# Performance work log

Hardware: AMD Instinct MI355X
Metric: run time of the kernel (lower is better)

Reference implementation:

```python
import jax, jax.numpy as jnp
import numpy as np

B, L, D = 4, 896, 2048
HQ, HKV, HD = 32, 8, 64
GROUP = HQ // HKV          # 4
TOKENS_PER_FRAME = 7
ROPE_BASE = 10000.0


def setup_inputs() -> dict:
    key = jax.random.key(0)
    ks = jax.random.split(key, 5)
    s = 0.02
    return {
        "x": jax.random.normal(ks[0], (B, L, D), jnp.float32),
        "wq": jax.random.normal(ks[1], (D, D), jnp.float32) * s,
        "wk": jax.random.normal(ks[2], (D, HKV * HD), jnp.float32) * s,
        "wv": jax.random.normal(ks[3], (D, HKV * HD), jnp.float32) * s,
        "wo": jax.random.normal(ks[4], (D, D), jnp.float32) * s,
        "pos_ids": jnp.arange(L, dtype=jnp.int32),
    }


def _apply_rotary(t, cos, sin):
    # t: [B, L, H, HD]; rotate all HD dims, interleaved pairs.
    Bt, Lt, Ht, Hd = t.shape
    tp = t.reshape(Bt, Lt, Ht, Hd // 2, 2)
    x1, x2 = tp[..., 0], tp[..., 1]
    c = cos[None, :, None, :]   # [1, L, 1, HD/2]
    s = sin[None, :, None, :]
    y1 = x1 * c - x2 * s
    y2 = x1 * s + x2 * c
    return jnp.stack([y1, y2], axis=-1).reshape(Bt, Lt, Ht, Hd)


def reference(x, wq, wk, wv, wo, pos_ids):
    Bx, Lx, Dx = x.shape
    q = (x @ wq).reshape(Bx, Lx, HQ, HD)
    k = (x @ wk).reshape(Bx, Lx, HKV, HD)
    v = (x @ wv).reshape(Bx, Lx, HKV, HD)

    # RoPE (rot_dim = head_dim), scale = 1.0
    half = HD // 2
    inv_freq = 1.0 / (ROPE_BASE ** (jnp.arange(half, dtype=jnp.float32) / half))
    freqs = pos_ids.astype(jnp.float32)[:, None] * inv_freq[None, :]  # [L, HD/2]
    cos, sin = jnp.cos(freqs), jnp.sin(freqs)
    q = _apply_rotary(q, cos, sin)
    k = _apply_rotary(k, cos, sin)

    # GQA: expand kv heads to q heads (kv_head = q_head // GROUP)
    k = jnp.repeat(k, GROUP, axis=2)   # [B, L, HQ, HD]
    v = jnp.repeat(v, GROUP, axis=2)

    scale = 1.0 / jnp.sqrt(jnp.float32(HD))
    scores = jnp.einsum('blhd,bmhd->bhlm', q, k) * scale  # [B, HQ, L, L]

    # frame-block causal mask: allow key frame <= query frame
    pos = jnp.arange(Lx)
    fid = pos // TOKENS_PER_FRAME
    allow = fid[None, :] <= fid[:, None]                  # [L, L]
    neg = jnp.finfo(scores.dtype).min
    scores = jnp.where(allow[None, None], scores, neg)

    probs = jax.nn.softmax(scores, axis=-1)
    out = jnp.einsum('bhlm,bmhd->blhd', probs, v).reshape(Bx, Lx, Dx)
    return out @ wo
```

## Files before the change

### kernel.cpp

```cpp
#include <hip/hip_runtime.h>
#include <hip/hip_bf16.h>
#include <cstdint>

typedef __bf16 bf16;
typedef __bf16 bf16x8 __attribute__((ext_vector_type(8)));
typedef float floatx4 __attribute__((ext_vector_type(4)));

#define B_   4
#define L_   896
#define D_   2048
#define HQ_  32
#define HKV_ 8
#define HD_  64
#define NQKV 3072
#define M_   3584

__device__ inline void gl_lds16(const bf16* g, bf16* l) {
    __builtin_amdgcn_global_load_lds(
        (const __attribute__((address_space(1))) void*)g,
        (__attribute__((address_space(3))) void*)l, 16, 0, 0);
}

__device__ inline void barrier_() {
    asm volatile("" ::: "memory");
    __builtin_amdgcn_s_barrier();
    asm volatile("" ::: "memory");
}

__global__ __launch_bounds__(256) void convert_to_bf16(const float* __restrict__ in,
                                                       bf16* __restrict__ out) {
    long q = (long)blockIdx.x * 256 + threadIdx.x;
    float4 v = ((const float4*)in)[q];
    union { bf16 b[4]; ushort4 u; } w;
    w.b[0] = (bf16)v.x; w.b[1] = (bf16)v.y; w.b[2] = (bf16)v.z; w.b[3] = (bf16)v.w;
    ((ushort4*)out)[q] = w.u;
}

__global__ __launch_bounds__(256) void rope_cs_kernel(const int* __restrict__ pos_ids,
                                                      float2* __restrict__ cs) {
    int idx = blockIdx.x * 256 + threadIdx.x;
    if (idx >= L_ * 32) return;
    int l = idx >> 5, i = idx & 31;
    float p = (float)pos_ids[l];
    float inv = exp2f(-(float)i * (13.287712379549449f / 32.0f));
    float a = p * inv;
    cs[idx] = make_float2(cosf(a), sinf(a));
}

__global__ __launch_bounds__(256) void rope_apply(bf16* __restrict__ QKV,
                                                  const float2* __restrict__ cs) {
    int idx = blockIdx.x * 256 + threadIdx.x;
    int m = idx / 320, g = idx - m * 320;
    int l = m % L_;
    int hp = (g * 4) & 31;
    const float2* ct = &cs[l * 32 + hp];
    bf16* p = QKV + (long)m * NQKV + g * 8;
    bf16x8 v = *(bf16x8*)p;
    bf16x8 w;
#pragma unroll
    for (int i = 0; i < 4; i++) {
        float2 csv = ct[i];
        float x1 = (float)v[2 * i], x2 = (float)v[2 * i + 1];
        w[2 * i]     = (bf16)(x1 * csv.x - x2 * csv.y);
        w[2 * i + 1] = (bf16)(x1 * csv.y + x2 * csv.x);
    }
    *(bf16x8*)p = w;
}

__global__ __launch_bounds__(256) void transpose_cvt(
    const float* __restrict__ in, ushort* __restrict__ out, int C, int R) {
    __shared__ ushort t[64][72];
    int tid = threadIdx.x;
    int tr = tid >> 4, tc = (tid & 15) << 2;
    long r0 = (long)blockIdx.y << 6, c0 = (long)blockIdx.x << 6;
#pragma unroll
    for (int i = 0; i < 4; ++i) {
        float4 v = *(const float4*)&in[(r0 + tr + i * 16) * C + c0 + tc];
        union { bf16 b[4]; ushort4 u; } w;
        w.b[0] = (bf16)v.x; w.b[1] = (bf16)v.y; w.b[2] = (bf16)v.z; w.b[3] = (bf16)v.w;
        *(ushort4*)&t[tr + i * 16][tc] = w.u;
    }
    __syncthreads();
#pragma unroll
    for (int i = 0; i < 4; ++i) {
        ushort4 w;
        w.x = t[tc + 0][tr + i * 16];
        w.y = t[tc + 1][tr + i * 16];
        w.z = t[tc + 2][tr + i * 16];
        w.w = t[tc + 3][tr + i * 16];
        *(ushort4*)&out[(c0 + tr + i * 16) * R + r0 + tc] = w;
    }
}

__global__ __launch_bounds__(256) void transpose_u16(
    const ushort* __restrict__ in, ushort* __restrict__ out,
    int ld_in, int ld_out, long is1, long is2, long os1, long os2) {
    __shared__ ushort t[64][72];
    int z = blockIdx.z;
    const ushort* ip = in + (long)(z >> 3) * is1 + (long)(z & 7) * is2;
    ushort* op = out + (long)(z >> 3) * os1 + (long)(z & 7) * os2;
    int tid = threadIdx.x;
    int tr = tid >> 4, tc = (tid & 15) << 2;
    long r0 = (long)blockIdx.y << 6, c0 = (long)blockIdx.x << 6;
#pragma unroll
    for (int i = 0; i < 4; ++i) {
        ushort4 v = *(const ushort4*)&ip[(r0 + tr + i * 16) * ld_in + c0 + tc];
        *(ushort4*)&t[tr + i * 16][tc] = v;
    }
    __syncthreads();
#pragma unroll
    for (int i = 0; i < 4; ++i) {
        ushort4 w;
        w.x = t[tc + 0][tr + i * 16];
        w.y = t[tc + 1][tr + i * 16];
        w.z = t[tc + 2][tr + i * 16];
        w.w = t[tc + 3][tr + i * 16];
        *(ushort4*)&op[(c0 + tr + i * 16) * ld_out + r0 + tc] = w;
    }
}

template <int JF, int OUTF32>
__global__ __launch_bounds__(512, 2) void gemm224(
    const bf16* __restrict__ A, const bf16* __restrict__ Bt, void* __restrict__ C,
    int Ntot, int Ktot) {
    __shared__ bf16 ldsA[2][224 * 64];
    __shared__ bf16 ldsB[2][JF * 64 * 64];
    const int tid = threadIdx.x;
    const int lane = tid & 63;
    const int quad = lane >> 4, l16 = lane & 15;
    const int w = tid >> 6;
    const int wr = w >> 2, wc = w & 3;

    const int gx = gridDim.x;
    const int nwg = gx * gridDim.y;
    int orig = blockIdx.y * gx + blockIdx.x;
    int q8 = nwg >> 3, r8 = nwg & 7;
    int xcd = orig & 7, lid = orig >> 3;
    int wg = (xcd < r8 ? xcd * (q8 + 1) : r8 * (q8 + 1) + (xcd - r8) * q8) + lid;
    const long m0 = (long)(wg / gx) * 224;
    const long n0 = (long)(wg % gx) * (JF * 64);

    const long rowK = Ktot;
    const int srow = tid >> 3;
    const int scol = ((tid & 7) ^ (srow & 7)) << 3;
    const bf16* baseA = A  + (m0 + srow) * rowK + scol;
    const bf16* baseB = Bt + (n0 + srow) * rowK + scol;
    bf16* const dA = (bf16*)ldsA + tid * 8;
    bf16* const dB = (bf16*)ldsB + tid * 8;

    const int m7 = l16 & 7;
    const int col0 = ((0 + quad) ^ m7) << 3;
    const int col1 = ((4 + quad) ^ m7) << 3;
    const int abase = wr * 112 + l16;
    const int bbase = wc * (JF * 16) + l16;

    floatx4 acc[7][JF];
#pragma unroll
    for (int i = 0; i < 7; ++i)
#pragma unroll
        for (int j = 0; j < JF; ++j)
#pragma unroll
            for (int r = 0; r < 4; ++r) acc[i][j][r] = 0.f;

    bf16x8 af0[4][2], af1[3][2], bq[JF][2];

    const int T = Ktot >> 6;

    {
        gl_lds16(baseA,              dA);
        gl_lds16(baseA + 64 * rowK,  dA + 4096);
        gl_lds16(baseA + 128 * rowK, dA + 8192);
        if (tid < 256) gl_lds16(baseA + 192 * rowK, dA + 12288);
#pragma unroll
        for (int r = 0; r < JF; ++r) gl_lds16(baseB + r * 64 * rowK, dB + r * 4096);
#pragma unroll
        for (int r = 0; r < JF; ++r) gl_lds16(baseB + 64 + r * 64 * rowK,
                                              dB + JF * 4096 + r * 4096);
    }
    if (JF == 3) asm volatile("s_waitcnt vmcnt(3)" ::: "memory");
    else         asm volatile("s_waitcnt vmcnt(2)" ::: "memory");
    barrier_();

    for (int t = 0; t < T; ++t) {
        const int cur = t & 1, nxt = cur ^ 1;
        const bf16* pa = &ldsA[cur][0];
        const bf16* pb = &ldsB[cur][0];
        const long koff  = (long)(t + 1) * 64;
        const long koff2 = (long)(t + 2) * 64;

#pragma unroll
        for (int i = 0; i < 4; ++i) {
            const bf16* rp = &pa[(abase + i * 16) * 64];
            af0[i][0] = *(const bf16x8*)&rp[col0];
            af0[i][1] = *(const bf16x8*)&rp[col1];
        }
#pragma unroll
        for (int j = 0; j < JF; ++j) {
            const bf16* rp = &pb[(bbase + j * 16) * 64];
            bq[j][0] = *(const bf16x8*)&rp[col0];
            bq[j][1] = *(const bf16x8*)&rp[col1];
        }
        if (t + 1 < T) {
            const bf16* g = baseA + koff;
            bf16* l = dA + nxt * (224 * 64);
            gl_lds16(g,              l);
            gl_lds16(g + 64 * rowK,  l + 4096);
            gl_lds16(g + 128 * rowK, l + 8192);
            if (tid < 256) gl_lds16(g + 192 * rowK, l + 12288);
        }
        barrier_();
        asm volatile("s_waitcnt lgkmcnt(0)" ::: "memory");
        __builtin_amdgcn_sched_barrier(0);
        __builtin_amdgcn_s_setprio(1);
#pragma unroll
        for (int i = 0; i < 4; ++i)
#pragma unroll
            for (int j = 0; j < JF; ++j) {
                floatx4 c = acc[i][j];
                c = __builtin_amdgcn_mfma_f32_16x16x32_bf16(af0[i][0], bq[j][0], c, 0, 0, 0);
                c = __builtin_amdgcn_mfma_f32_16x16x32_bf16(af0[i][1], bq[j][1], c, 0, 0, 0);
                acc[i][j] = c;
            }
        __builtin_amdgcn_s_setprio(0);
        barrier_();

#pragma unroll
        for (int i = 0; i < 3; ++i) {
            const bf16* rp = &pa[(abase + (4 + i) * 16) * 64];
            af1[i][0] = *(const bf16x8*)&rp[col0];
            af1[i][1] = *(const bf16x8*)&rp[col1];
        }
        if (t + 2 < T) {
            const bf16* g = baseB + koff2;
            bf16* l = dB + cur * (JF * 64 * 64);
#pragma unroll
            for (int r = 0; r < JF; ++r) gl_lds16(g + r * 64 * rowK, l + r * 4096);
        }
        barrier_();
        asm volatile("s_waitcnt lgkmcnt(0)" ::: "memory");
        __builtin_amdgcn_sched_barrier(0);
        __builtin_amdgcn_s_setprio(1);
#pragma unroll
        for (int i = 0; i < 3; ++i)
#pragma unroll
            for (int j = 0; j < JF; ++j) {
                floatx4 c = acc[4 + i][j];
                c = __builtin_amdgcn_mfma_f32_16x16x32_bf16(af1[i][0], bq[j][0], c, 0, 0, 0);
                c = __builtin_amdgcn_mfma_f32_16x16x32_bf16(af1[i][1], bq[j][1], c, 0, 0, 0);
                acc[4 + i][j] = c;
            }
        __builtin_amdgcn_s_setprio(0);
        if (t + 2 < T) {
            if (JF == 3) asm volatile("s_waitcnt vmcnt(3)" ::: "memory");
            else         asm volatile("s_waitcnt vmcnt(2)" ::: "memory");
        } else {
            asm volatile("s_waitcnt vmcnt(0)" ::: "memory");
        }
        barrier_();
    }

#pragma unroll
    for (int i = 0; i < 7; ++i)
#pragma unroll
        for (int j = 0; j < JF; ++j)
#pragma unroll
            for (int r = 0; r < 4; ++r) {
                long m = m0 + wr * 112 + i * 16 + quad * 4 + r;
                long n = n0 + wc * (JF * 16) + j * 16 + l16;
                if (OUTF32) ((float*)C)[m * Ntot + n] = acc[i][j][r];
                else        ((bf16*)C)[m * Ntot + n] = (bf16)acc[i][j][r];
            }
}

__global__ __launch_bounds__(256) void attn_kernel(
    const bf16* __restrict__ QKV,
    const bf16* __restrict__ Vt,
    bf16* __restrict__ AO) {
    __shared__ bf16 Ks[64 * 72];
    __shared__ bf16 Vs[64 * 72];
    __shared__ bf16 Ps[4][64 * 72];
    const int tid  = threadIdx.x;
    const int wid  = tid >> 6, lane = tid & 63;
    const int quad = lane >> 4, c = lane & 15;
    const int b = blockIdx.z, kvh = blockIdx.y;
    const int hq = kvh * 4 + wid;
    const int q0b = blockIdx.x * 64;
    bf16* ps = &Ps[wid][0];

    const bf16* Qb = QKV + ((long)(b * L_ + q0b)) * NQKV + hq * HD_;
    const bf16* Kb = QKV + ((long)(b * L_)) * NQKV + D_ + kvh * HD_;
    const bf16* Vb = Vt + ((long)(b * HKV_ + kvh)) * (HD_ * L_);

    bf16x8 qf[4][2];
#pragma unroll
    for (int a = 0; a < 4; a++) {
        qf[a][0] = *(const bf16x8*)&Qb[(long)(a * 16 + c) * NQKV + quad * 8];
        qf[a][1] = *(const bf16x8*)&Qb[(long)(a * 16 + c) * NQKV + 32 + quad * 8];
    }

    float lsum[4][4];
    floatx4 o[4][4];
#pragma unroll
    for (int a = 0; a < 4; a++)
#pragma unroll
        for (int r = 0; r < 4; r++) lsum[a][r] = 0.f;
#pragma unroll
    for (int a = 0; a < 4; a++)
#pragma unroll
        for (int nt = 0; nt < 4; nt++)
#pragma unroll
            for (int r = 0; r < 4; r++) o[a][nt][r] = 0.f;

    int fe[4][4];
#pragma unroll
    for (int a = 0; a < 4; a++)
#pragma unroll
        for (int r = 0; r < 4; r++) {
            int l = q0b + a * 16 + quad * 4 + r;
            fe[a][r] = (l / 7 + 1) * 7;
        }
    const int kend = ((q0b + 63) / 7 + 1) * 7;

    const int srow = tid >> 3, schunk = (tid & 7) << 3;

    for (int k0 = 0; k0 < kend; k0 += 64) {
        bf16x8 kg0 = *(const bf16x8*)&Kb[(long)(k0 + srow) * NQKV + schunk];
        bf16x8 kg1 = *(const bf16x8*)&Kb[(long)(k0 + 32 + srow) * NQKV + schunk];
        bf16x8 vg0 = *(const bf16x8*)&Vb[(long)srow * L_ + k0 + schunk];
        bf16x8 vg1 = *(const bf16x8*)&Vb[(long)(srow + 32) * L_ + k0 + schunk];
        __syncthreads();
        *(bf16x8*)&Ks[srow * 72 + schunk]        = kg0;
        *(bf16x8*)&Ks[(srow + 32) * 72 + schunk] = kg1;
        *(bf16x8*)&Vs[srow * 72 + schunk]        = vg0;
        *(bf16x8*)&Vs[(srow + 32) * 72 + schunk] = vg1;
        __syncthreads();

        bf16x8 kf[4][2];
#pragma unroll
        for (int n = 0; n < 4; n++) {
            kf[n][0] = *(bf16x8*)&Ks[(n * 16 + c) * 72 + quad * 8];
            kf[n][1] = *(bf16x8*)&Ks[(n * 16 + c) * 72 + 32 + quad * 8];
        }
#pragma unroll
        for (int a = 0; a < 4; a++) {
            floatx4 s[4];
#pragma unroll
            for (int n = 0; n < 4; n++) {
#pragma unroll
                for (int r = 0; r < 4; r++) s[n][r] = 0.f;
                s[n] = __builtin_amdgcn_mfma_f32_16x16x32_bf16(qf[a][0], kf[n][0], s[n], 0, 0, 0);
                s[n] = __builtin_amdgcn_mfma_f32_16x16x32_bf16(qf[a][1], kf[n][1], s[n], 0, 0, 0);
            }
#pragma unroll
            for (int n = 0; n < 4; n++) {
                const int key = k0 + n * 16 + c;
#pragma unroll
                for (int r = 0; r < 4; r++) {
                    float e = __expf(fmaf(s[n][r], 0.125f, -12.0f));
                    e = (key < fe[a][r]) ? e : 0.f;
                    lsum[a][r] += e;
                    ps[(a * 16 + quad * 4 + r) * 72 + n * 16 + c] = (bf16)e;
                }
            }
        }
        bf16x8 vf[4][2];
#pragma unroll
        for (int nt = 0; nt < 4; nt++) {
            vf[nt][0] = *(bf16x8*)&Vs[(nt * 16 + c) * 72 + quad * 8];
            vf[nt][1] = *(bf16x8*)&Vs[(nt * 16 + c) * 72 + 32 + quad * 8];
        }
#pragma unroll
        for (int a = 0; a < 4; a++) {
            bf16x8 pf0 = *(bf16x8*)&ps[(a * 16 + c) * 72 + quad * 8];
            bf16x8 pf1 = *(bf16x8*)&ps[(a * 16 + c) * 72 + 32 + quad * 8];
#pragma unroll
            for (int nt = 0; nt < 4; nt++) {
                o[a][nt] = __builtin_amdgcn_mfma_f32_16x16x32_bf16(pf0, vf[nt][0], o[a][nt], 0, 0, 0);
                o[a][nt] = __builtin_amdgcn_mfma_f32_16x16x32_bf16(pf1, vf[nt][1], o[a][nt], 0, 0, 0);
            }
        }
    }
#pragma unroll
    for (int a = 0; a < 4; a++)
#pragma unroll
        for (int r = 0; r < 4; r++) {
#pragma unroll
            for (int off = 1; off < 16; off <<= 1) lsum[a][r] += __shfl_xor(lsum[a][r], off);
        }
#pragma unroll
    for (int a = 0; a < 4; a++)
#pragma unroll
        for (int nt = 0; nt < 4; nt++)
#pragma unroll
            for (int r = 0; r < 4; r++) {
                int l = q0b + a * 16 + quad * 4 + r;
                AO[((long)(b * L_ + l)) * D_ + hq * HD_ + nt * 16 + c] =
                    (bf16)(o[a][nt][r] / lsum[a][r]);
            }
}

extern "C" void kernel_launch(void* const* d_in, const int* in_sizes, int n_in,
                              void* d_out, int out_size, void* d_ws, size_t ws_size,
                              hipStream_t stream) {
    (void)in_sizes; (void)n_in; (void)out_size; (void)ws_size;
    const float* x  = (const float*)d_in[0];
    const float* wq = (const float*)d_in[1];
    const float* wk = (const float*)d_in[2];
    const float* wv = (const float*)d_in[3];
    const float* wo = (const float*)d_in[4];
    const int* pos  = (const int*)d_in[5];

    bf16* ws    = (bf16*)d_ws;
    bf16* xb    = ws;
    bf16* wqkvT = ws + 7340032L;
    bf16* woT   = ws + 13631488L;
    bf16* QKV   = ws + 17825792L;
    bf16* Vt    = ws + 28835840L;
    bf16* AO    = xb;
    float2* cs  = (float2*)(ws + 30670848L);

    convert_to_bf16<<<dim3(7168), 256, 0, stream>>>(x, xb);
    rope_cs_kernel<<<dim3(112), dim3(256), 0, stream>>>(pos, cs);

    transpose_cvt<<<dim3(32, 32), 256, 0, stream>>>(wq, (ushort*)wqkvT, 2048, 2048);
    transpose_cvt<<<dim3(8, 32), 256, 0, stream>>>(wk, (ushort*)(wqkvT + 4194304L), 512, 2048);
    transpose_cvt<<<dim3(8, 32), 256, 0, stream>>>(wv, (ushort*)(wqkvT + 5242880L), 512, 2048);
    transpose_cvt<<<dim3(32, 32), 256, 0, stream>>>(wo, (ushort*)woT, 2048, 2048);

    gemm224<3, 0><<<dim3(16, 16), 512, 0, stream>>>(xb, wqkvT, QKV, NQKV, D_);

    rope_apply<<<dim3(4480), 256, 0, stream>>>(QKV, cs);

    transpose_u16<<<dim3(1, 14, 32), 256, 0, stream>>>(
        (const ushort*)(QKV + 2560), (ushort*)Vt, 3072, 896,
        896L * 3072, 64, 8L * 57344, 57344);

    attn_kernel<<<dim3(14, 8, 4), 256, 0, stream>>>(QKV, Vt, AO);

    gemm224<2, 1><<<dim3(16, 16), 512, 0, stream>>>(AO, woT, d_out, D_, D_);
}
```

Baseline: 268.3 us.

## Rebalance causal attention by pairing query tiles per block with prefetch and mask skip

Each block now handles two query tiles, x and 13-x, in sequence so causal work is balanced across blocks. It uses 8 waves of 512 threads, each wave covering 32 query rows. The next K/V tile is loaded into registers while the current one is computed. Mask evaluation is skipped for key tiles that lie fully below the frame boundary, and exp2 with a folded scale replaces expf with a constant shift. The grid halves to 224 blocks, which may leave CUs underused, and dropping the stabilizing shift slightly raises overflow risk.

```diff
diff --git a/kernel.cpp b/kernel.cpp
--- a/kernel.cpp
+++ b/kernel.cpp
@@ -272,131 +272,159 @@
             }
 }
 
-__global__ __launch_bounds__(256) void attn_kernel(
+__global__ __launch_bounds__(512) void attn_kernel(
     const bf16* __restrict__ QKV,
     const bf16* __restrict__ Vt,
     bf16* __restrict__ AO) {
     __shared__ bf16 Ks[64 * 72];
     __shared__ bf16 Vs[64 * 72];
-    __shared__ bf16 Ps[4][64 * 72];
+    __shared__ bf16 Ps[8][32 * 72];
     const int tid  = threadIdx.x;
     const int wid  = tid >> 6, lane = tid & 63;
     const int quad = lane >> 4, c = lane & 15;
     const int b = blockIdx.z, kvh = blockIdx.y;
-    const int hq = kvh * 4 + wid;
-    const int q0b = blockIdx.x * 64;
+    const int hq = kvh * 4 + (wid >> 1);
+    const int sub = wid & 1;
+    const int xpair = blockIdx.x;
     bf16* ps = &Ps[wid][0];
 
-    const bf16* Qb = QKV + ((long)(b * L_ + q0b)) * NQKV + hq * HD_;
     const bf16* Kb = QKV + ((long)(b * L_)) * NQKV + D_ + kvh * HD_;
     const bf16* Vb = Vt + ((long)(b * HKV_ + kvh)) * (HD_ * L_);
 
-    bf16x8 qf[4][2];
-#pragma unroll
-    for (int a = 0; a < 4; a++) {
-        qf[a][0] = *(const bf16x8*)&Qb[(long)(a * 16 + c) * NQKV + quad * 8];
-        qf[a][1] = *(const bf16x8*)&Qb[(long)(a * 16 + c) * NQKV + 32 + quad * 8];
-    }
-
-    float lsum[4][4];
-    floatx4 o[4][4];
-#pragma unroll
-    for (int a = 0; a < 4; a++)
-#pragma unroll
-        for (int r = 0; r < 4; r++) lsum[a][r] = 0.f;
-#pragma unroll
-    for (int a = 0; a < 4; a++)
-#pragma unroll
-        for (int nt = 0; nt < 4; nt++)
-#pragma unroll
-            for (int r = 0; r < 4; r++) o[a][nt][r] = 0.f;
-
-    int fe[4][4];
-#pragma unroll
-    for (int a = 0; a < 4; a++)
-#pragma unroll
-        for (int r = 0; r < 4; r++) {
-            int l = q0b + a * 16 + quad * 4 + r;
-            fe[a][r] = (l / 7 + 1) * 7;
-        }
-    const int kend = ((q0b + 63) / 7 + 1) * 7;
-
     const int srow = tid >> 3, schunk = (tid & 7) << 3;
-
-    for (int k0 = 0; k0 < kend; k0 += 64) {
-        bf16x8 kg0 = *(const bf16x8*)&Kb[(long)(k0 + srow) * NQKV + schunk];
-        bf16x8 kg1 = *(const bf16x8*)&Kb[(long)(k0 + 32 + srow) * NQKV + schunk];
-        bf16x8 vg0 = *(const bf16x8*)&Vb[(long)srow * L_ + k0 + schunk];
-        bf16x8 vg1 = *(const bf16x8*)&Vb[(long)(srow + 32) * L_ + k0 + schunk];
-        __syncthreads();
-        *(bf16x8*)&Ks[srow * 72 + schunk]        = kg0;
-        *(bf16x8*)&Ks[(srow + 32) * 72 + schunk] = kg1;
-        *(bf16x8*)&Vs[srow * 72 + schunk]        = vg0;
-        *(bf16x8*)&Vs[(srow + 32) * 72 + schunk] = vg1;
-        __syncthreads();
-
-        bf16x8 kf[4][2];
-#pragma unroll
-        for (int n = 0; n < 4; n++) {
-            kf[n][0] = *(bf16x8*)&Ks[(n * 16 + c) * 72 + quad * 8];
-            kf[n][1] = *(bf16x8*)&Ks[(n * 16 + c) * 72 + 32 + quad * 8];
-        }
-#pragma unroll
-        for (int a = 0; a < 4; a++) {
-            floatx4 s[4];
+    const bf16* kp = &Kb[(long)srow * NQKV + schunk];
+    const bf16* vp = &Vb[(long)srow * L_ + schunk];
+
+    const floatx4 fzero = {0.f, 0.f, 0.f, 0.f};
+    const float C1 = 0.18033688011112042f;
+
+#pragma unroll 1
+    for (int pass = 0; pass < 2; ++pass) {
+        const int x = pass == 0 ? xpair : 13 - xpair;
+        const int q0b = x * 64;
+        const bf16* Qb = QKV + ((long)(b * L_ + q0b + sub * 32)) * NQKV + hq * HD_;
+
+        bf16x8 qf[2][2];
+#pragma unroll
+        for (int a = 0; a < 2; a++) {
+            qf[a][0] = *(const bf16x8*)&Qb[(long)(a * 16 + c) * NQKV + quad * 8];
+            qf[a][1] = *(const bf16x8*)&Qb[(long)(a * 16 + c) * NQKV + 32 + quad * 8];
+        }
+
+        float lsum[2][4];
+        floatx4 o[2][4];
+#pragma unroll
+        for (int a = 0; a < 2; a++)
+#pragma unroll
+            for (int r = 0; r < 4; r++) lsum[a][r] = 0.f;
+#pragma unroll
+        for (int a = 0; a < 2; a++)
+#pragma unroll
+            for (int nt = 0; nt < 4; nt++)
+#pragma unroll
+                for (int r = 0; r < 4; r++) o[a][nt][r] = 0.f;
+
+        int fe[2][4];
+#pragma unroll
+        for (int a = 0; a < 2; a++)
+#pragma unroll
+            for (int r = 0; r < 4; r++) {
+                int l = q0b + sub * 32 + a * 16 + quad * 4 + r;
+                fe[a][r] = (l / 7 + 1) * 7;
+            }
+        const int femin = (q0b / 7 + 1) * 7;
+        const int kend  = ((q0b + 63) / 7 + 1) * 7;
+
+        bf16x8 kg = *(const bf16x8*)&kp[0];
+        bf16x8 vg = *(const bf16x8*)&vp[0];
+
+        for (int k0 = 0; k0 < kend; k0 += 64) {
+            __syncthreads();
+            *(bf16x8*)&Ks[srow * 72 + schunk] = kg;
+            *(bf16x8*)&Vs[srow * 72 + schunk] = vg;
+            __syncthreads();
+
+            const int kn = k0 + 64;
+            if (kn < kend) {
+                kg = *(const bf16x8*)&kp[(long)kn * NQKV];
+                vg = *(const bf16x8*)&vp[kn];
+            }
+
+            bf16x8 kf[4][2];
 #pragma unroll
             for (int n = 0; n < 4; n++) {
-#pragma unroll
-                for (int r = 0; r < 4; r++) s[n][r] = 0.f;
-                s[n] = __builtin_amdgcn_mfma_f32_16x16x32_bf16(qf[a][0], kf[n][0], s[n], 0, 0, 0);
-                s[n] = __builtin_amdgcn_mfma_f32_16x16x32_bf16(qf[a][1], kf[n][1], s[n], 0, 0, 0);
-            }
-#pragma unroll
-            for (int n = 0; n < 4; n++) {
-                const int key = k0 + n * 16 + c;
+                kf[n][0] = *(bf16x8*)&Ks[(n * 16 + c) * 72 + quad * 8];
+                kf[n][1] = *(bf16x8*)&Ks[(n * 16 + c) * 72 + 32 + quad * 8];
+            }
+            const int masked = (k0 + 64 > femin);
+#pragma unroll
+            for (int a = 0; a < 2; a++) {
+                floatx4 s[4];
+#pragma unroll
+                for (int n = 0; n < 4; n++) {
+                    s[n] = __builtin_amdgcn_mfma_f32_16x16x32_bf16(qf[a][0], kf[n][0], fzero, 0, 0, 0);
+                    s[n] = __builtin_amdgcn_mfma_f32_16x16x32_bf16(qf[a][1], kf[n][1], s[n], 0, 0, 0);
+                }
+                if (masked) {
+#pragma unroll
+                    for (int n = 0; n < 4; n++) {
+                        const int key = k0 + n * 16 + c;
+#pragma unroll
+                        for (int r = 0; r < 4; r++) {
+                            float e = exp2f(s[n][r] * C1);
+                            e = (key < fe[a][r]) ? e : 0.f;
+                            lsum[a][r] += e;
+                            ps[(a * 16 + quad * 4 + r) * 72 + n * 16 + c] = (bf16)e;
+                        }
+                    }
+                } else {
+#pragma unroll
+                    for (int n = 0; n < 4; n++) {
+#pragma unroll
+                        for (int r = 0; r < 4; r++) {
+                            float e = exp2f(s[n][r] * C1);
+                            lsum[a][r] += e;
+                            ps[(a * 16 + quad * 4 + r) * 72 + n * 16 + c] = (bf16)e;
+                        }
+                    }
+                }
+            }
+            bf16x8 vf[4][2];
+#pragma unroll
+            for (int nt = 0; nt < 4; nt++) {
+                vf[nt][0] = *(bf16x8*)&Vs[(nt * 16 + c) * 72 + quad * 8];
+                vf[nt][1] = *(bf16x8*)&Vs[(nt * 16 + c) * 72 + 32 + quad * 8];
+            }
+#pragma unroll
+            for (int a = 0; a < 2; a++) {
+                bf16x8 pf0 = *(bf16x8*)&ps[(a * 16 + c) * 72 + quad * 8];
+                bf16x8 pf1 = *(bf16x8*)&ps[(a * 16 + c) * 72 + 32 + quad * 8];
+#pragma unroll
+                for (int nt = 0; nt < 4; nt++) {
+                    o[a][nt] = __builtin_amdgcn_mfma_f32_16x16x32_bf16(pf0, vf[nt][0], o[a][nt], 0, 0, 0);
+                    o[a][nt] = __builtin_amdgcn_mfma_f32_16x16x32_bf16(pf1, vf[nt][1], o[a][nt], 0, 0, 0);
+                }
+            }
+        }
+#pragma unroll
+        for (int a = 0; a < 2; a++)
+#pragma unroll
+            for (int r = 0; r < 4; r++) {
+#pragma unroll
+                for (int off = 1; off < 16; off <<= 1)
+                    lsum[a][r] += __shfl_xor(lsum[a][r], off);
+            }
+#pragma unroll
+        for (int a = 0; a < 2; a++)
+#pragma unroll
+            for (int nt = 0; nt < 4; nt++)
 #pragma unroll
                 for (int r = 0; r < 4; r++) {
-                    float e = __expf(fmaf(s[n][r], 0.125f, -12.0f));
-                    e = (key < fe[a][r]) ? e : 0.f;
-                    lsum[a][r] += e;
-                    ps[(a * 16 + quad * 4 + r) * 72 + n * 16 + c] = (bf16)e;
+                    int l = q0b + sub * 32 + a * 16 + quad * 4 + r;
+                    AO[((long)(b * L_ + l)) * D_ + hq * HD_ + nt * 16 + c] =
+                        (bf16)(o[a][nt][r] / lsum[a][r]);
                 }
-            }
-        }
-        bf16x8 vf[4][2];
-#pragma unroll
-        for (int nt = 0; nt < 4; nt++) {
-            vf[nt][0] = *(bf16x8*)&Vs[(nt * 16 + c) * 72 + quad * 8];
-            vf[nt][1] = *(bf16x8*)&Vs[(nt * 16 + c) * 72 + 32 + quad * 8];
-        }
-#pragma unroll
-        for (int a = 0; a < 4; a++) {
-            bf16x8 pf0 = *(bf16x8*)&ps[(a * 16 + c) * 72 + quad * 8];
-            bf16x8 pf1 = *(bf16x8*)&ps[(a * 16 + c) * 72 + 32 + quad * 8];
-#pragma unroll
-            for (int nt = 0; nt < 4; nt++) {
-                o[a][nt] = __builtin_amdgcn_mfma_f32_16x16x32_bf16(pf0, vf[nt][0], o[a][nt], 0, 0, 0);
-                o[a][nt] = __builtin_amdgcn_mfma_f32_16x16x32_bf16(pf1, vf[nt][1], o[a][nt], 0, 0, 0);
-            }
-        }
-    }
-#pragma unroll
-    for (int a = 0; a < 4; a++)
-#pragma unroll
-        for (int r = 0; r < 4; r++) {
-#pragma unroll
-            for (int off = 1; off < 16; off <<= 1) lsum[a][r] += __shfl_xor(lsum[a][r], off);
-        }
-#pragma unroll
-    for (int a = 0; a < 4; a++)
-#pragma unroll
-        for (int nt = 0; nt < 4; nt++)
-#pragma unroll
-            for (int r = 0; r < 4; r++) {
-                int l = q0b + a * 16 + quad * 4 + r;
-                AO[((long)(b * L_ + l)) * D_ + hq * HD_ + nt * 16 + c] =
-                    (bf16)(o[a][nt][r] / lsum[a][r]);
-            }
+    }
 }
 
 extern "C" void kernel_launch(void* const* d_in, const int* in_sizes, int n_in,
@@ -435,7 +463,7 @@
         (const ushort*)(QKV + 2560), (ushort*)Vt, 3072, 896,
         896L * 3072, 64, 8L * 57344, 57344);
 
-    attn_kernel<<<dim3(14, 8, 4), 256, 0, stream>>>(QKV, Vt, AO);
+    attn_kernel<<<dim3(7, 8, 4), 512, 0, stream>>>(QKV, Vt, AO);
 
     gemm224<2, 1><<<dim3(16, 16), 512, 0, stream>>>(AO, woT, d_out, D_, D_);
 }
```

Measured after the change: 258.9 us. 3.5% less time.
